# Kernel tuning notes

Measured on AMD Instinct MI355X. Metric: run time of the kernel, lower is better.

Reference implementation:

```python
import jax, jax.numpy as jnp
import numpy as np
from jax import lax

EPS = 1e-5
DN = ('NCHW', 'OIHW', 'NCHW')

def ternarize(w):
    # TWN-style ternarization: delta = 0.7*mean|w|, alpha = mean of |w| above threshold
    a = jnp.abs(w)
    delta = 0.7 * jnp.mean(a)
    mask = (a > delta).astype(w.dtype)
    alpha = jnp.sum(a * mask) / jnp.maximum(jnp.sum(mask), 1.0)
    return alpha * jnp.sign(w) * mask

def conv(x, w, stride=1, pad=0, groups=1):
    return lax.conv_general_dilated(
        x, w, (stride, stride), [(pad, pad), (pad, pad)],
        feature_group_count=groups, dimension_numbers=DN)

def batchnorm(x, gamma, beta):
    # training-mode BN: per-channel batch statistics over (N,H,W)
    mean = jnp.mean(x, axis=(0, 2, 3), keepdims=True)
    var = jnp.var(x, axis=(0, 2, 3), keepdims=True)
    inv = lax.rsqrt(var + EPS)
    return (x - mean) * inv * gamma[None, :, None, None] + beta[None, :, None, None]

def setup_inputs() -> dict:
    key = jax.random.key(0)
    ks = jax.random.split(key, 10)
    B, Cin, H, W = 32, 96, 56, 56
    planes, Cout = 576, 96
    return {
        'x':  jax.random.normal(ks[0], (B, Cin, H, W), jnp.float32),
        'w1': jax.random.normal(ks[1], (planes, Cin, 1, 1), jnp.float32) * 0.1,
        'g1': jax.random.uniform(ks[2], (planes,), jnp.float32, 0.5, 1.5),
        'b1': jax.random.normal(ks[3], (planes,), jnp.float32) * 0.1,
        'w2': jax.random.normal(ks[4], (planes, 1, 3, 3), jnp.float32) * 0.1,
        'g2': jax.random.uniform(ks[5], (planes,), jnp.float32, 0.5, 1.5),
        'b2': jax.random.normal(ks[6], (planes,), jnp.float32) * 0.1,
        'w3': jax.random.normal(ks[7], (Cout, planes, 1, 1), jnp.float32) * 0.1,
        'g3': jax.random.uniform(ks[8], (Cout,), jnp.float32, 0.5, 1.5),
        'b3': jax.random.normal(ks[9], (Cout,), jnp.float32) * 0.1,
    }

def reference(x, w1, g1, b1, w2, g2, b2, w3, g3, b3):
    planes = w1.shape[0]
    # expand 1x1 (ternary) + BN + ReLU
    out = jax.nn.relu(batchnorm(conv(x, ternarize(w1)), g1, b1))
    # depthwise 3x3 stride 1 (ternary) + BN + ReLU
    out = jax.nn.relu(batchnorm(conv(out, ternarize(w2), stride=1, pad=1, groups=planes), g2, b2))
    # project 1x1 (ternary) + BN
    out = batchnorm(conv(out, ternarize(w3)), g3, b3)
    # stride==1 and in_planes==out_planes -> identity shortcut
    return out + x
```

## Files before the change

kernel.cpp:

```cpp
#include <hip/hip_runtime.h>
#include <hip/hip_bf16.h>

#define BATCH 32
#define CIN 96
#define HW 3136
#define PL 576
#define COUT 96
#define NT 49
#define NHW 100352.0

typedef __attribute__((ext_vector_type(4))) float f32x4;
typedef __attribute__((ext_vector_type(8))) short s16x8;

__device__ __forceinline__ unsigned short f2b(float v) {
  __hip_bfloat16 h = __float2bfloat16(v);
  return *reinterpret_cast<unsigned short*>(&h);
}
__device__ __forceinline__ float b2f(unsigned int u) {
  return __uint_as_float((u & 0xffffu) << 16);
}

__global__ __launch_bounds__(256) void absred_kernel(const float* __restrict__ w,
                                                     float* __restrict__ part, int n4) {
  __shared__ float ra[256];
  const int tid = threadIdx.x;
  float s = 0.f;
  for (int i = blockIdx.x * 256 + tid; i < n4; i += 32 * 256) {
    float4 v = reinterpret_cast<const float4*>(w)[i];
    s += fabsf(v.x) + fabsf(v.y) + fabsf(v.z) + fabsf(v.w);
  }
  ra[tid] = s; __syncthreads();
  for (int off = 128; off; off >>= 1) { if (tid < off) ra[tid] += ra[tid + off]; __syncthreads(); }
  if (tid == 0) part[blockIdx.x] = ra[0];
}

__device__ __forceinline__ float delta_from_parts(const float* __restrict__ part, float invn) {
  float s = 0.f;
#pragma unroll
  for (int i = 0; i < 32; ++i) s += part[i];
  return 0.7f * s * invn;
}

__global__ __launch_bounds__(256) void ternw_bf16_kernel(
    const float* __restrict__ w, const float* __restrict__ part, float invn,
    __hip_bfloat16* __restrict__ tw, int n4) {
  const float delta = delta_from_parts(part, invn);
  const int i = blockIdx.x * 256 + threadIdx.x;
  if (i >= n4) return;
  float4 v = reinterpret_cast<const float4*>(w)[i];
  float vv[4] = {v.x, v.y, v.z, v.w};
  unsigned short b[4];
#pragma unroll
  for (int j = 0; j < 4; ++j)
    b[j] = (fabsf(vv[j]) > delta)
               ? (unsigned short)(0x3F80u | ((__float_as_uint(vv[j]) >> 16) & 0x8000u))
               : (unsigned short)0;
  unsigned lo = (unsigned)b[0] | ((unsigned)b[1] << 16);
  unsigned hi = (unsigned)b[2] | ((unsigned)b[3] << 16);
  reinterpret_cast<uint2*>(tw)[i] = make_uint2(lo, hi);
}

__global__ __launch_bounds__(256) void ternw_f32_kernel(
    const float* __restrict__ w, const float* __restrict__ part, float invn,
    float* __restrict__ tw, int n4) {
  const float delta = delta_from_parts(part, invn);
  const int i = blockIdx.x * 256 + threadIdx.x;
  if (i >= n4) return;
  float4 v = reinterpret_cast<const float4*>(w)[i];
  float4 o;
  o.x = (fabsf(v.x) > delta) ? (v.x > 0.f ? 1.f : -1.f) : 0.f;
  o.y = (fabsf(v.y) > delta) ? (v.y > 0.f ? 1.f : -1.f) : 0.f;
  o.z = (fabsf(v.z) > delta) ? (v.z > 0.f ? 1.f : -1.f) : 0.f;
  o.w = (fabsf(v.w) > delta) ? (v.w > 0.f ? 1.f : -1.f) : 0.f;
  reinterpret_cast<float4*>(tw)[i] = o;
}

__global__ __launch_bounds__(256) void bnp_kernel(
    const float* __restrict__ psum, const float* __restrict__ psumsq,
    const float* __restrict__ gamma, const float* __restrict__ beta,
    float* __restrict__ sc, float* __restrict__ sh, int nparts) {
  const int ch = blockIdx.x, tid = threadIdx.x;
  double s = 0.0, q = 0.0;
  for (int i = tid; i < nparts; i += 256) {
    s += (double)psum[(size_t)ch * nparts + i];
    q += (double)psumsq[(size_t)ch * nparts + i];
  }
  __shared__ double rs[256], rq[256];
  rs[tid] = s; rq[tid] = q; __syncthreads();
  for (int off = 128; off; off >>= 1) {
    if (tid < off) { rs[tid] += rs[tid + off]; rq[tid] += rq[tid + off]; }
    __syncthreads();
  }
  if (tid == 0) {
    double mean = rs[0] / NHW;
    double var = rq[0] / NHW - mean * mean;
    float inv = (float)(1.0 / sqrt(var + 1e-5));
    float g = gamma[ch];
    sc[ch] = inv * g;
    sh[ch] = beta[ch] - (float)mean * inv * g;
  }
}

__global__ __launch_bounds__(256) void conv1_mfma(
    const float* __restrict__ x, const __hip_bfloat16* __restrict__ tw1,
    __hip_bfloat16* __restrict__ o1c,
    float* __restrict__ psum, float* __restrict__ psumsq) {
  __shared__ __hip_bfloat16 Bt[64 * 104];
  __shared__ __hip_bfloat16 ot[64 * 200];
  const int hwt = blockIdx.x, n = blockIdx.y, mt = blockIdx.z;
  const int t0 = hwt * 64;
  const int tid = threadIdx.x;
  const int lane = tid & 63, w = tid >> 6;

  {
    const float* xp = x + (size_t)n * CIN * HW + t0 + lane;
    const int cb = w * 24;
#pragma unroll
    for (int i6 = 0; i6 < 6; ++i6) {
      const int c0 = cb + i6 * 4;
      float v0 = xp[(size_t)(c0 + 0) * HW];
      float v1 = xp[(size_t)(c0 + 1) * HW];
      float v2 = xp[(size_t)(c0 + 2) * HW];
      float v3 = xp[(size_t)(c0 + 3) * HW];
      unsigned lo = (unsigned)f2b(v0) | ((unsigned)f2b(v1) << 16);
      unsigned hi = (unsigned)f2b(v2) | ((unsigned)f2b(v3) << 16);
      *reinterpret_cast<uint2*>(&Bt[lane * 104 + c0]) = make_uint2(lo, hi);
    }
  }
  __syncthreads();

  const int l15 = lane & 15, lh = lane >> 4;
  f32x4 acc[3][4];
#pragma unroll
  for (int f = 0; f < 3; ++f)
#pragma unroll
    for (int g = 0; g < 4; ++g) acc[f][g] = (f32x4){0.f, 0.f, 0.f, 0.f};
  const int rowb = mt * 192 + w * 48;
#pragma unroll
  for (int k0 = 0; k0 < 3; ++k0) {
    s16x8 a[3], b[4];
#pragma unroll
    for (int f = 0; f < 3; ++f)
      a[f] = *reinterpret_cast<const s16x8*>(tw1 + (size_t)(rowb + f * 16 + l15) * CIN + k0 * 32 + lh * 8);
#pragma unroll
    for (int g = 0; g < 4; ++g)
      b[g] = *reinterpret_cast<const s16x8*>(&Bt[(g * 16 + l15) * 104 + k0 * 32 + lh * 8]);
#pragma unroll
    for (int f = 0; f < 3; ++f)
#pragma unroll
      for (int g = 0; g < 4; ++g)
        acc[f][g] = __builtin_amdgcn_mfma_f32_16x16x32_bf16(a[f], b[g], acc[f][g], 0, 0, 0);
  }

#pragma unroll
  for (int f = 0; f < 3; ++f) {
    float sred[4] = {0.f, 0.f, 0.f, 0.f};
    float qred[4] = {0.f, 0.f, 0.f, 0.f};
    const int ch0 = rowb + f * 16 + lh * 4;
#pragma unroll
    for (int g = 0; g < 4; ++g)
#pragma unroll
      for (int r = 0; r < 4; ++r) {
        float v = acc[f][g][r];
        sred[r] += v; qred[r] = fmaf(v, v, qred[r]);
      }
#pragma unroll
    for (int r = 0; r < 4; ++r) {
      float s = sred[r], q = qred[r];
#pragma unroll
      for (int m = 1; m < 16; m <<= 1) { s += __shfl_xor(s, m); q += __shfl_xor(q, m); }
      if (l15 == 0) {
        const int pi = (ch0 + r) * 1568 + n * NT + hwt;
        psum[pi] = s; psumsq[pi] = q;
      }
    }
  }

#pragma unroll
  for (int f = 0; f < 3; ++f) {
    const int chL = w * 48 + f * 16 + lh * 4;
#pragma unroll
    for (int g = 0; g < 4; ++g) {
      unsigned p0 = (unsigned)f2b(acc[f][g][0]) | ((unsigned)f2b(acc[f][g][1]) << 16);
      unsigned p1 = (unsigned)f2b(acc[f][g][2]) | ((unsigned)f2b(acc[f][g][3]) << 16);
      *reinterpret_cast<uint2*>(&ot[(g * 16 + l15) * 200 + chL]) = make_uint2(p0, p1);
    }
  }
  __syncthreads();

  {
    const int hwp = tid >> 3, q = tid & 7;
#pragma unroll
    for (int half = 0; half < 2; ++half) {
      const int hw = half * 32 + hwp;
      const __hip_bfloat16* srcp = &ot[hw * 200];
      __hip_bfloat16* dst = o1c + ((size_t)n * HW + t0 + hw) * PL + mt * 192;
#pragma unroll
      for (int s = 0; s < 3; ++s) {
        const int c8 = q + s * 8;
        *reinterpret_cast<uint4*>(dst + c8 * 8) =
            *reinterpret_cast<const uint4*>(srcp + c8 * 8);
      }
    }
  }
}

__global__ __launch_bounds__(64) void dw_kernel(
    const __hip_bfloat16* __restrict__ o1c, const float* __restrict__ tw2,
    const float* __restrict__ s1, const float* __restrict__ t1,
    __hip_bfloat16* __restrict__ o2c,
    float* __restrict__ psum, float* __restrict__ psumsq) {
  const int strip = blockIdx.x, kh = blockIdx.y, n = blockIdx.z;
  const int lane = threadIdx.x;
  const int col = lane >> 4, chs = lane & 15;
  const int c = strip * 4 + col;
  const int chb = kh * 64 + chs * 4;
  const int ec = (col == 0) ? (c - 1) : (c + 1);
  const bool eok = (col == 0) ? (c > 0) : ((col == 3) ? (c < 55) : false);

  float sc[4], sh[4], wt[9][4];
#pragma unroll
  for (int j = 0; j < 4; ++j) {
    sc[j] = s1[chb + j]; sh[j] = t1[chb + j];
#pragma unroll
    for (int t = 0; t < 9; ++t) wt[t][j] = tw2[(chb + j) * 9 + t];
  }

  const size_t nb = (size_t)n * HW;
  const __hip_bfloat16* pc = o1c + (nb + c) * PL + chb;
  const __hip_bfloat16* pe = o1c + (nb + ((eok ? ec : c))) * PL + chb;
  __hip_bfloat16* po = o2c + (nb + c) * PL + chb;

  uint2 rc[8], re[8];
  float Wl[4][4], Wc[4][4], Wr[4][4];
  float psc[4] = {0.f, 0.f, 0.f, 0.f}, psq[4] = {0.f, 0.f, 0.f, 0.f};

#define LOADRAW(s, q_) do {                                                    \
    rc[s] = make_uint2(0u, 0u); re[s] = make_uint2(0u, 0u);                    \
    if ((q_) < 56) {                                                           \
      rc[s] = *reinterpret_cast<const uint2*>(pc + (size_t)(q_) * 56 * PL);    \
      if (eok) re[s] = *reinterpret_cast<const uint2*>(pe + (size_t)(q_) * 56 * PL); \
    } } while (0)

#define BN4(dst, raw) do {                                                     \
    dst[0] = fmaxf(fmaf(b2f((raw).x), sc[0], sh[0]), 0.f);                     \
    dst[1] = fmaxf(fmaf(b2f((raw).x >> 16), sc[1], sh[1]), 0.f);               \
    dst[2] = fmaxf(fmaf(b2f((raw).y), sc[2], sh[2]), 0.f);                     \
    dst[3] = fmaxf(fmaf(b2f((raw).y >> 16), sc[3], sh[3]), 0.f);               \
  } while (0)

#define CONVW(wi, s, q_) do {                                                  \
    if ((q_) < 56) {                                                           \
      float cen_[4], ee_[4];                                                   \
      BN4(cen_, rc[s]); BN4(ee_, re[s]);                                       \
      _Pragma("unroll")                                                        \
      for (int j = 0; j < 4; ++j) {                                            \
        float lv = __shfl(cen_[j], lane - 16);                                 \
        float rv = __shfl(cen_[j], lane + 16);                                 \
        float ev = eok ? ee_[j] : 0.f;                                         \
        Wc[wi][j] = cen_[j];                                                   \
        Wl[wi][j] = (col == 0) ? ev : lv;                                      \
        Wr[wi][j] = (col == 3) ? ev : rv;                                      \
      }                                                                        \
    } else {                                                                   \
      _Pragma("unroll")                                                        \
      for (int j = 0; j < 4; ++j) { Wl[wi][j] = 0.f; Wc[wi][j] = 0.f; Wr[wi][j] = 0.f; } \
    } } while (0)

#define COMPW(qm, q0, qp, q_) do {                                             \
    float o_[4];                                                               \
    _Pragma("unroll")                                                          \
    for (int j = 0; j < 4; ++j) {                                              \
      float a_ = wt[0][j] * Wl[qm][j];                                         \
      a_ = fmaf(wt[1][j], Wc[qm][j], a_);                                      \
      a_ = fmaf(wt[2][j], Wr[qm][j], a_);                                      \
      a_ = fmaf(wt[3][j], Wl[q0][j], a_);                                      \
      a_ = fmaf(wt[4][j], Wc[q0][j], a_);                                      \
      a_ = fmaf(wt[5][j], Wr[q0][j], a_);                                      \
      a_ = fmaf(wt[6][j], Wl[qp][j], a_);                                      \
      a_ = fmaf(wt[7][j], Wc[qp][j], a_);                                      \
      a_ = fmaf(wt[8][j], Wr[qp][j], a_);                                      \
      o_[j] = a_;                                                              \
      psc[j] += a_; psq[j] = fmaf(a_, a_, psq[j]);                             \
    }                                                                          \
    unsigned pk0 = (unsigned)f2b(o_[0]) | ((unsigned)f2b(o_[1]) << 16);        \
    unsigned pk1 = (unsigned)f2b(o_[2]) | ((unsigned)f2b(o_[3]) << 16);        \
    *reinterpret_cast<uint2*>(po + (size_t)(q_) * 56 * PL) = make_uint2(pk0, pk1); \
  } while (0)

  LOADRAW(0, 0); LOADRAW(1, 1); LOADRAW(2, 2); LOADRAW(3, 3);
  LOADRAW(4, 4); LOADRAW(5, 5); LOADRAW(6, 6); LOADRAW(7, 7);
  CONVW(0, 0, 0);
#pragma unroll
  for (int j = 0; j < 4; ++j) { Wl[3][j] = 0.f; Wc[3][j] = 0.f; Wr[3][j] = 0.f; }

  for (int t = 0; t < 7; ++t) {
    const int q = 8 * t;
    LOADRAW(0, q + 8);  CONVW(1, 1, q + 1);  COMPW(3, 0, 1, q);
    LOADRAW(1, q + 9);  CONVW(2, 2, q + 2);  COMPW(0, 1, 2, q + 1);
    LOADRAW(2, q + 10); CONVW(3, 3, q + 3);  COMPW(1, 2, 3, q + 2);
    LOADRAW(3, q + 11); CONVW(0, 4, q + 4);  COMPW(2, 3, 0, q + 3);
    LOADRAW(4, q + 12); CONVW(1, 5, q + 5);  COMPW(3, 0, 1, q + 4);
    LOADRAW(5, q + 13); CONVW(2, 6, q + 6);  COMPW(0, 1, 2, q + 5);
    LOADRAW(6, q + 14); CONVW(3, 7, q + 7);  COMPW(1, 2, 3, q + 6);
    LOADRAW(7, q + 15); CONVW(0, 0, q + 8);  COMPW(2, 3, 0, q + 7);
  }
#undef COMPW
#undef CONVW
#undef BN4
#undef LOADRAW

#pragma unroll
  for (int j = 0; j < 4; ++j) {
    psc[j] += __shfl_xor(psc[j], 16); psc[j] += __shfl_xor(psc[j], 32);
    psq[j] += __shfl_xor(psq[j], 16); psq[j] += __shfl_xor(psq[j], 32);
  }
  if (col == 0) {
#pragma unroll
    for (int j = 0; j < 4; ++j) {
      const int pi = (chb + j) * 448 + n * 14 + strip;
      psum[pi] = psc[j]; psumsq[pi] = psq[j];
    }
  }
}

__global__ __launch_bounds__(256) void conv3_mfma(
    const __hip_bfloat16* __restrict__ o2c, const __hip_bfloat16* __restrict__ tw3,
    const float* __restrict__ s2, const float* __restrict__ t2,
    __hip_bfloat16* __restrict__ out3,
    float* __restrict__ psum, float* __restrict__ psumsq) {
  __shared__ alignas(16) char shraw[9 * 8192];
  __shared__ float s2s[PL], t2s[PL];
  float* smem = reinterpret_cast<float*>(shraw);
  const int hwt = blockIdx.x, n = blockIdx.y, tid = threadIdx.x;
  const int lane = tid & 63, w = tid >> 6;
  const int l15 = lane & 15, lh = lane >> 4;
  const int wm = w >> 1, wn = w & 1;
  const int t0 = hwt * 64;
  for (int i = tid; i < PL; i += 256) { s2s[i] = s2[i]; t2s[i] = t2[i]; }

  const int hwp = tid >> 2;
  const int cq = tid & 3;
  const __hip_bfloat16* src = o2c + ((size_t)n * HW + t0 + hwp) * PL + cq * 16;
  uint4 ra[9], rb[9];
#pragma unroll
  for (int kc = 0; kc < 9; ++kc) {
    ra[kc] = *reinterpret_cast<const uint4*>(src + kc * 64);
    rb[kc] = *reinterpret_cast<const uint4*>(src + kc * 64 + 8);
  }
  __syncthreads();

  const unsigned key = (unsigned)((hwp & 7) << 4);
#pragma unroll
  for (int kc = 0; kc < 9; ++kc) {
    const int cb16 = kc * 64 + cq * 16;
    unsigned uu[8] = {ra[kc].x, ra[kc].y, ra[kc].z, ra[kc].w,
                      rb[kc].x, rb[kc].y, rb[kc].z, rb[kc].w};
    unsigned po[8];
#pragma unroll
    for (int j = 0; j < 8; ++j) {
      float lo = fmaxf(fmaf(b2f(uu[j]),       s2s[cb16 + 2 * j],     t2s[cb16 + 2 * j]), 0.f);
      float hi = fmaxf(fmaf(b2f(uu[j] >> 16), s2s[cb16 + 2 * j + 1], t2s[cb16 + 2 * j + 1]), 0.f);
      po[j] = (unsigned)f2b(lo) | ((unsigned)f2b(hi) << 16);
    }
    char* base = shraw + kc * 8192 + hwp * 128;
    *reinterpret_cast<uint4*>(base + (((unsigned)(cq * 32)) ^ key)) =
        make_uint4(po[0], po[1], po[2], po[3]);
    *reinterpret_cast<uint4*>(base + (((unsigned)(cq * 32 + 16)) ^ key)) =
        make_uint4(po[4], po[5], po[6], po[7]);
  }
  __syncthreads();

  f32x4 acc[3][2];
#pragma unroll
  for (int f = 0; f < 3; ++f)
#pragma unroll
    for (int g = 0; g < 2; ++g) acc[f][g] = (f32x4){0.f, 0.f, 0.f, 0.f};

#pragma unroll
  for (int kc = 0; kc < 9; ++kc) {
#pragma unroll
    for (int kb = 0; kb < 2; ++kb) {
      s16x8 a[3];
#pragma unroll
      for (int f = 0; f < 3; ++f)
        a[f] = *reinterpret_cast<const s16x8*>(
            tw3 + (size_t)(wm * 48 + f * 16 + l15) * PL + kc * 64 + kb * 32 + lh * 8);
#pragma unroll
      for (int g = 0; g < 2; ++g) {
        const int row = wn * 32 + g * 16 + l15;
        const unsigned cbyte = (unsigned)(kb * 64 + lh * 16) ^ (unsigned)((row & 7) << 4);
        const s16x8 b = *reinterpret_cast<const s16x8*>(
            shraw + kc * 8192 + row * 128 + cbyte);
#pragma unroll
        for (int f = 0; f < 3; ++f)
          acc[f][g] = __builtin_amdgcn_mfma_f32_16x16x32_bf16(a[f], b, acc[f][g], 0, 0, 0);
      }
    }
  }
  __syncthreads();
#pragma unroll
  for (int f = 0; f < 3; ++f)
#pragma unroll
    for (int g = 0; g < 2; ++g)
#pragma unroll
      for (int r = 0; r < 4; ++r)
        smem[(wm * 48 + f * 16 + lh * 4 + r) * 65 + wn * 32 + g * 16 + l15] = acc[f][g][r];
  __syncthreads();
  const int slot = tid & 7, rgrp = tid >> 3;
#pragma unroll
  for (int s = 0; s < 3; ++s) {
    const int rl = s * 32 + rgrp;
    float v[8], sm = 0.f, sq = 0.f;
#pragma unroll
    for (int j = 0; j < 8; ++j) {
      float t = smem[rl * 65 + slot * 8 + j];
      v[j] = t; sm += t; sq = fmaf(t, t, sq);
    }
    unsigned pk[4];
#pragma unroll
    for (int j = 0; j < 4; ++j) pk[j] = (unsigned)f2b(v[2 * j]) | ((unsigned)f2b(v[2 * j + 1]) << 16);
    *reinterpret_cast<uint4*>(out3 + ((size_t)n * COUT + rl) * HW + t0 + slot * 8) =
        make_uint4(pk[0], pk[1], pk[2], pk[3]);
#pragma unroll
    for (int m = 1; m < 8; m <<= 1) { sm += __shfl_xor(sm, m, 8); sq += __shfl_xor(sq, m, 8); }
    if (slot == 0) { int pi = rl * 1568 + n * NT + hwt; psum[pi] = sm; psumsq[pi] = sq; }
  }
}

__global__ __launch_bounds__(256) void final_kernel(
    const __hip_bfloat16* __restrict__ out3, const float* __restrict__ x,
    const float* __restrict__ s3, const float* __restrict__ t3,
    float* __restrict__ out) {
  const int i = blockIdx.x * 256 + threadIdx.x;
  const int p = (i * 4) / HW;
  const int co = p - (p / COUT) * COUT;
  uint2 raw = reinterpret_cast<const uint2*>(out3)[i];
  float4 b = reinterpret_cast<const float4*>(x)[i];
  const float scv = s3[co], tv = t3[co];
  float4 r;
  r.x = fmaf(b2f(raw.x), scv, tv) + b.x;
  r.y = fmaf(b2f(raw.x >> 16), scv, tv) + b.y;
  r.z = fmaf(b2f(raw.y), scv, tv) + b.z;
  r.w = fmaf(b2f(raw.y >> 16), scv, tv) + b.w;
  reinterpret_cast<float4*>(out)[i] = r;
}

extern "C" void kernel_launch(void* const* d_in, const int* in_sizes, int n_in,
                              void* d_out, int out_size, void* d_ws, size_t ws_size,
                              hipStream_t stream) {
  const float* x  = (const float*)d_in[0];
  const float* w1 = (const float*)d_in[1];
  const float* g1 = (const float*)d_in[2];
  const float* b1 = (const float*)d_in[3];
  const float* w2 = (const float*)d_in[4];
  const float* g2 = (const float*)d_in[5];
  const float* b2 = (const float*)d_in[6];
  const float* w3 = (const float*)d_in[7];
  const float* g3 = (const float*)d_in[8];
  const float* b3 = (const float*)d_in[9];
  float* out = (float*)d_out;

  char* ws = (char*)d_ws;
  __hip_bfloat16* tw1b = (__hip_bfloat16*)(ws + 0);
  __hip_bfloat16* tw3b = (__hip_bfloat16*)(ws + 110592);
  float* tw2f = (float*)(ws + 221184);
  float* s1 = (float*)(ws + 241920);
  float* t1 = s1 + PL; float* s2 = t1 + PL; float* t2 = s2 + PL;
  float* s3 = (float*)(ws + 251136); float* t3 = s3 + COUT;
  float* ps1 = (float*)(ws + 251904);
  float* pq1 = ps1 + PL * 1568;
  float* ps2 = pq1 + PL * 1568;
  float* pq2 = ps2 + PL * 1568;
  float* ps3 = pq2 + PL * 1568;
  float* pq3 = ps3 + COUT * 1568;
  float* part1 = pq3 + COUT * 1568;
  float* part2 = part1 + 32;
  float* part3 = part2 + 32;
  __hip_bfloat16* o1c = (__hip_bfloat16*)(ws + 16777216);
  __hip_bfloat16* o2c = o1c + (size_t)BATCH * HW * PL;
  __hip_bfloat16* out3b = o1c;

  absred_kernel<<<32, 256, 0, stream>>>(w1, part1, 13824);
  absred_kernel<<<32, 256, 0, stream>>>(w2, part2, 1296);
  absred_kernel<<<32, 256, 0, stream>>>(w3, part3, 13824);
  ternw_bf16_kernel<<<54, 256, 0, stream>>>(w1, part1, 1.0f / 55296.0f, tw1b, 13824);
  ternw_f32_kernel <<<6, 256, 0, stream>>>(w2, part2, 1.0f / 5184.0f, tw2f, 1296);
  ternw_bf16_kernel<<<54, 256, 0, stream>>>(w3, part3, 1.0f / 55296.0f, tw3b, 13824);

  conv1_mfma<<<dim3(NT, BATCH, 3), 256, 0, stream>>>(x, tw1b, o1c, ps1, pq1);
  bnp_kernel<<<PL, 256, 0, stream>>>(ps1, pq1, g1, b1, s1, t1, 1568);

  dw_kernel<<<dim3(14, 9, BATCH), 64, 0, stream>>>(o1c, tw2f, s1, t1, o2c, ps2, pq2);
  bnp_kernel<<<PL, 256, 0, stream>>>(ps2, pq2, g2, b2, s2, t2, 448);

  conv3_mfma<<<dim3(NT, BATCH), 256, 0, stream>>>(o2c, tw3b, s2, t2, out3b, ps3, pq3);
  bnp_kernel<<<COUT, 256, 0, stream>>>(ps3, pq3, g3, b3, s3, t3, 1568);

  final_kernel<<<out_size / 1024, 256, 0, stream>>>(out3b, x, s3, t3, out);
}
```

Baseline: 234.6 us.

## Double-buffer conv3 LDS staging and overlap global prefetch with MFMA

The conv3 kernel used to load all nine K-chunks into registers, stage them into 72KB of LDS, and only then run the MFMA loop. It now keeps a four-slot register prefetch ring and a two-buffer 32KB LDS ring. BN2+ReLU staging of later chunks is interleaved with MFMA on earlier chunks, with global prefetches issued ahead. The aim is to cut LDS use so more blocks fit per CU, to lower register pressure, and to hide global latency behind compute. The cost is extra __syncthreads barriers.

Result: faster. 228.2 us (-2.7%).

```diff
diff --git a/kernel.cpp b/kernel.cpp
--- a/kernel.cpp
+++ b/kernel.cpp
@@ -329,7 +329,7 @@
     const float* __restrict__ s2, const float* __restrict__ t2,
     __hip_bfloat16* __restrict__ out3,
     float* __restrict__ psum, float* __restrict__ psumsq) {
-  __shared__ alignas(16) char shraw[9 * 8192];
+  __shared__ alignas(16) char shraw[32768];
   __shared__ float s2s[PL], t2s[PL];
   float* smem = reinterpret_cast<float*>(shraw);
   const int hwt = blockIdx.x, n = blockIdx.y, tid = threadIdx.x;
@@ -342,62 +342,88 @@
   const int hwp = tid >> 2;
   const int cq = tid & 3;
   const __hip_bfloat16* src = o2c + ((size_t)n * HW + t0 + hwp) * PL + cq * 16;
-  uint4 ra[9], rb[9];
-#pragma unroll
-  for (int kc = 0; kc < 9; ++kc) {
-    ra[kc] = *reinterpret_cast<const uint4*>(src + kc * 64);
-    rb[kc] = *reinterpret_cast<const uint4*>(src + kc * 64 + 8);
-  }
-  __syncthreads();
+  uint4 qa[4], qb[4];
+#pragma unroll
+  for (int c = 0; c < 4; ++c) {
+    qa[c] = *reinterpret_cast<const uint4*>(src + c * 64);
+    qb[c] = *reinterpret_cast<const uint4*>(src + c * 64 + 8);
+  }
+
+  f32x4 acc[3][2];
+#pragma unroll
+  for (int f = 0; f < 3; ++f)
+#pragma unroll
+    for (int g = 0; g < 2; ++g) acc[f][g] = (f32x4){0.f, 0.f, 0.f, 0.f};
 
   const unsigned key = (unsigned)((hwp & 7) << 4);
-#pragma unroll
-  for (int kc = 0; kc < 9; ++kc) {
-    const int cb16 = kc * 64 + cq * 16;
-    unsigned uu[8] = {ra[kc].x, ra[kc].y, ra[kc].z, ra[kc].w,
-                      rb[kc].x, rb[kc].y, rb[kc].z, rb[kc].w};
-    unsigned po[8];
-#pragma unroll
-    for (int j = 0; j < 8; ++j) {
-      float lo = fmaxf(fmaf(b2f(uu[j]),       s2s[cb16 + 2 * j],     t2s[cb16 + 2 * j]), 0.f);
-      float hi = fmaxf(fmaf(b2f(uu[j] >> 16), s2s[cb16 + 2 * j + 1], t2s[cb16 + 2 * j + 1]), 0.f);
-      po[j] = (unsigned)f2b(lo) | ((unsigned)f2b(hi) << 16);
-    }
-    char* base = shraw + kc * 8192 + hwp * 128;
-    *reinterpret_cast<uint4*>(base + (((unsigned)(cq * 32)) ^ key)) =
-        make_uint4(po[0], po[1], po[2], po[3]);
-    *reinterpret_cast<uint4*>(base + (((unsigned)(cq * 32 + 16)) ^ key)) =
-        make_uint4(po[4], po[5], po[6], po[7]);
-  }
-  __syncthreads();
-
-  f32x4 acc[3][2];
-#pragma unroll
-  for (int f = 0; f < 3; ++f)
-#pragma unroll
-    for (int g = 0; g < 2; ++g) acc[f][g] = (f32x4){0.f, 0.f, 0.f, 0.f};
-
-#pragma unroll
-  for (int kc = 0; kc < 9; ++kc) {
-#pragma unroll
-    for (int kb = 0; kb < 2; ++kb) {
-      s16x8 a[3];
-#pragma unroll
-      for (int f = 0; f < 3; ++f)
-        a[f] = *reinterpret_cast<const s16x8*>(
-            tw3 + (size_t)(wm * 48 + f * 16 + l15) * PL + kc * 64 + kb * 32 + lh * 8);
-#pragma unroll
-      for (int g = 0; g < 2; ++g) {
-        const int row = wn * 32 + g * 16 + l15;
-        const unsigned cbyte = (unsigned)(kb * 64 + lh * 16) ^ (unsigned)((row & 7) << 4);
-        const s16x8 b = *reinterpret_cast<const s16x8*>(
-            shraw + kc * 8192 + row * 128 + cbyte);
-#pragma unroll
-        for (int f = 0; f < 3; ++f)
-          acc[f][g] = __builtin_amdgcn_mfma_f32_16x16x32_bf16(a[f], b, acc[f][g], 0, 0, 0);
-      }
-    }
-  }
+  __syncthreads();
+
+#define STAGE(kc, s, pb, half) do {                                            \
+    const int cb16 = (kc) * 64 + cq * 16;                                      \
+    unsigned uu[8] = {qa[s].x, qa[s].y, qa[s].z, qa[s].w,                      \
+                      qb[s].x, qb[s].y, qb[s].z, qb[s].w};                     \
+    unsigned po[8];                                                            \
+    _Pragma("unroll")                                                          \
+    for (int j = 0; j < 8; ++j) {                                              \
+      float lo = fmaxf(fmaf(b2f(uu[j]),       s2s[cb16 + 2 * j],     t2s[cb16 + 2 * j]), 0.f); \
+      float hi = fmaxf(fmaf(b2f(uu[j] >> 16), s2s[cb16 + 2 * j + 1], t2s[cb16 + 2 * j + 1]), 0.f); \
+      po[j] = (unsigned)f2b(lo) | ((unsigned)f2b(hi) << 16);                   \
+    }                                                                          \
+    char* base = shraw + (pb) * 16384 + (half) * 8192 + hwp * 128;             \
+    *reinterpret_cast<uint4*>(base + (((unsigned)(cq * 32)) ^ key)) =          \
+        make_uint4(po[0], po[1], po[2], po[3]);                                \
+    *reinterpret_cast<uint4*>(base + (((unsigned)(cq * 32 + 16)) ^ key)) =     \
+        make_uint4(po[4], po[5], po[6], po[7]);                                \
+  } while (0)
+
+#define PREF(kc, s) do {                                                       \
+    qa[s] = *reinterpret_cast<const uint4*>(src + (kc) * 64);                  \
+    qb[s] = *reinterpret_cast<const uint4*>(src + (kc) * 64 + 8);              \
+  } while (0)
+
+#define MF(kc, pb, half) do {                                                  \
+    _Pragma("unroll")                                                          \
+    for (int kb = 0; kb < 2; ++kb) {                                           \
+      s16x8 a_[3];                                                             \
+      _Pragma("unroll")                                                        \
+      for (int f = 0; f < 3; ++f)                                              \
+        a_[f] = *reinterpret_cast<const s16x8*>(                               \
+            tw3 + (size_t)(wm * 48 + f * 16 + l15) * PL + (kc) * 64 + kb * 32 + lh * 8); \
+      _Pragma("unroll")                                                        \
+      for (int g = 0; g < 2; ++g) {                                            \
+        const int row = wn * 32 + g * 16 + l15;                                \
+        const unsigned cbyte = (unsigned)(kb * 64 + lh * 16) ^ (unsigned)((row & 7) << 4); \
+        const s16x8 b_ = *reinterpret_cast<const s16x8*>(                      \
+            shraw + (pb) * 16384 + (half) * 8192 + row * 128 + cbyte);         \
+        _Pragma("unroll")                                                      \
+        for (int f = 0; f < 3; ++f)                                            \
+          acc[f][g] = __builtin_amdgcn_mfma_f32_16x16x32_bf16(a_[f], b_, acc[f][g], 0, 0, 0); \
+      }                                                                        \
+    }                                                                          \
+  } while (0)
+
+  STAGE(0, 0, 0, 0); STAGE(1, 1, 0, 1);
+  __syncthreads();
+  PREF(4, 0); PREF(5, 1);
+  MF(0, 0, 0); MF(1, 0, 1);
+  STAGE(2, 2, 1, 0); STAGE(3, 3, 1, 1);
+  __syncthreads();
+  PREF(6, 2); PREF(7, 3);
+  MF(2, 1, 0); MF(3, 1, 1);
+  STAGE(4, 0, 0, 0); STAGE(5, 1, 0, 1);
+  __syncthreads();
+  PREF(8, 0);
+  MF(4, 0, 0); MF(5, 0, 1);
+  STAGE(6, 2, 1, 0); STAGE(7, 3, 1, 1);
+  __syncthreads();
+  MF(6, 1, 0); MF(7, 1, 1);
+  STAGE(8, 0, 0, 0);
+  __syncthreads();
+  MF(8, 0, 0);
+#undef MF
+#undef PREF
+#undef STAGE
+
   __syncthreads();
 #pragma unroll
   for (int f = 0; f < 3; ++f)
```
